# Kernel tuning notes

Measured on AMD Instinct MI355X. Metric: run time of the kernel, lower is better.

The kernel has to match this reference:

```python
import jax, jax.numpy as jnp
import numpy as np

B = 64          # batch_size
N_PER = 1000    # num_nodes per graph
NTOT = B * N_PER
H = 64          # hidden_gnn_dim


def _gcn_aggregate(x, senders, receivers, add_self_edges):
    """jraph.GraphConvolution aggregation with symmetric normalization.
    x: [NTOT, F] node features AFTER update_node_fn."""
    if add_self_edges:
        self_idx = jnp.arange(NTOT, dtype=senders.dtype)
        s = jnp.concatenate([senders, self_idx])
        r = jnp.concatenate([receivers, self_idx])
    else:
        s, r = senders, receivers
    ones = jnp.ones_like(s, dtype=x.dtype)
    deg_s = jax.ops.segment_sum(ones, s, num_segments=NTOT)
    deg_r = jax.ops.segment_sum(ones, r, num_segments=NTOT)
    x = x * jax.lax.rsqrt(jnp.maximum(deg_s, 1.0))[:, None]
    x = jax.ops.segment_sum(x[s], r, num_segments=NTOT)
    x = x * jax.lax.rsqrt(jnp.maximum(deg_r, 1.0))[:, None]
    return x


def setup_inputs() -> dict:
    key = jax.random.key(0)
    ks = jax.random.split(key, 12)
    n_edges = 1_000_000
    in_dim, fc, lat, out_dim = 64, 512, 64, 32
    flat = N_PER * H  # 64000

    def w(k, shape, fan_in):
        return jax.random.normal(k, shape, dtype=jnp.float32) / np.sqrt(fan_in)

    return {
        "nodes": jax.random.normal(ks[0], (NTOT, in_dim), dtype=jnp.float32),
        "senders": jax.random.randint(ks[1], (n_edges,), 0, NTOT),
        "receivers": jax.random.randint(ks[2], (n_edges,), 0, NTOT),
        "eps": jax.random.normal(ks[3], (B, lat), dtype=jnp.float32),
        "W_gcn1": w(ks[4], (in_dim, H), in_dim),
        "b_gcn1": jnp.zeros((H,), jnp.float32),
        "W_fc": w(ks[5], (flat, fc), flat),
        "b_fc": jnp.zeros((fc,), jnp.float32),
        "W_mean": w(ks[6], (fc, lat), fc),
        "b_mean": jnp.zeros((lat,), jnp.float32),
        "W_logstd": w(ks[7], (fc, lat), fc),
        "b_logstd": jnp.zeros((lat,), jnp.float32),
        "W_dec_fc": w(ks[8], (lat, flat), lat),
        "b_dec_fc": jnp.zeros((flat,), jnp.float32),
        "W_dec_out": w(ks[9], (H, out_dim), H),
        "b_dec_out": jnp.zeros((out_dim,), jnp.float32),
    }


def reference(nodes, senders, receivers, eps, W_gcn1, b_gcn1, W_fc, b_fc,
              W_mean, b_mean, W_logstd, b_logstd, W_dec_fc, b_dec_fc,
              W_dec_out, b_dec_out):
    # --- Encoder: GCN(update=Linear+relu, add_self_edges=True) ---
    h = jax.nn.relu(nodes @ W_gcn1 + b_gcn1)                 # [NTOT, H]
    h = _gcn_aggregate(h, senders, receivers, add_self_edges=True)
    x = h.reshape(B, N_PER * H)                              # flatten per graph
    x = jax.nn.relu(x @ W_fc + b_fc)                         # [B, fc]
    mean = x @ W_mean + b_mean                               # [B, lat]
    log_std = x @ W_logstd + b_logstd                        # [B, lat]
    # --- Reparameterization ---
    z = mean + jnp.exp(log_std) * eps                        # [B, lat]
    # --- Decoder ---
    d = jax.nn.relu(z @ W_dec_fc + b_dec_fc)                 # [B, N_PER*H]
    d = d.reshape(NTOT, H)
    d = d @ W_dec_out + b_dec_out                            # update_node_fn
    out_nodes = _gcn_aggregate(d, senders, receivers, add_self_edges=False)
    return mean, log_std, out_nodes
```

## Files before the change

### kernel.cpp

```cpp
#include <hip/hip_runtime.h>
#include <math.h>

#define NTOT 64000
#define HD   64
#define NB   64
#define FC   512
#define LAT  64
#define OUTD 32
#define GKC  256
#define NKB  250
#define NBH  64
#define NBUK 250
#define BSH  8

typedef __bf16 bf16x8 __attribute__((ext_vector_type(8)));
typedef float  f32x4  __attribute__((ext_vector_type(4)));

__device__ inline float bflo(unsigned u) { union {unsigned q; float f;} x; x.q = u << 16; return x.f; }
__device__ inline float bfhi(unsigned u) { union {unsigned q; float f;} x; x.q = u & 0xFFFF0000u; return x.f; }
__device__ inline unsigned pkbf(float lo, float hi) {
  __bf16 a = (__bf16)lo, b = (__bf16)hi;
  unsigned short ua, ub;
  __builtin_memcpy(&ua, &a, 2); __builtin_memcpy(&ub, &b, 2);
  return (unsigned)ua | ((unsigned)ub << 16);
}

__global__ __launch_bounds__(256) void k_hist(const int* __restrict__ s,
    const int* __restrict__ r, unsigned* __restrict__ partials, int nE) {
  __shared__ unsigned hist[16000];
  int arr = blockIdx.y;
  const int* idx = arr ? r : s;
  unsigned* base = partials + ((size_t)arr * NBH + blockIdx.x) * 16000;
  for (int u = threadIdx.x; u < 16000; u += 256) hist[u] = 0;
  __syncthreads();
  int chunk = (nE + NBH - 1) / NBH;
  int e0 = blockIdx.x * chunk;
  int e1 = min(e0 + chunk, nE);
  for (int e = e0 + threadIdx.x; e < e1; e += 256) {
    int i = idx[e];
    atomicAdd(&hist[i >> 2], 1u << ((i & 3) * 8));
  }
  __syncthreads();
  for (int u = threadIdx.x; u < 16000; u += 256) base[u] = hist[u];
}

__global__ __launch_bounds__(128) void k_sum(const unsigned* __restrict__ partials,
    int* __restrict__ dout, int* __restrict__ din) {
  int t = blockIdx.x * 128 + threadIdx.x;
  unsigned a = 0, b = 0;
  for (int bk = 0; bk < NBH; bk++) {
    a += partials[(size_t)bk * 16000 + t];
    b += partials[((size_t)NBH + bk) * 16000 + t];
  }
  int4 va = make_int4(a & 255, (a >> 8) & 255, (a >> 16) & 255, a >> 24);
  int4 vb = make_int4(b & 255, (b >> 8) & 255, (b >> 16) & 255, b >> 24);
  *reinterpret_cast<int4*>(dout + t * 4) = va;
  *reinterpret_cast<int4*>(din + t * 4) = vb;
}

__global__ void k_scan1(const int* __restrict__ din, int* __restrict__ rs,
                        int* __restrict__ bsums) {
  __shared__ int sm[256];
  int i = blockIdx.x * 256 + threadIdx.x;
  int v = din[i];
  sm[threadIdx.x] = v;
  __syncthreads();
  for (int d = 1; d < 256; d <<= 1) {
    int t = (threadIdx.x >= d) ? sm[threadIdx.x - d] : 0;
    __syncthreads();
    sm[threadIdx.x] += t;
    __syncthreads();
  }
  rs[i] = sm[threadIdx.x] - v;
  if (threadIdx.x == 255) bsums[blockIdx.x] = sm[255];
}

__global__ void k_scan2(int* __restrict__ rs, int* __restrict__ gcur,
                        const int* __restrict__ bsums, int nE) {
  __shared__ int sm[256];
  int bid = blockIdx.x, t = threadIdx.x;
  sm[t] = (t < bid) ? bsums[t] : 0;
  __syncthreads();
  for (int d = 128; d > 0; d >>= 1) {
    if (t < d) sm[t] += sm[t + d];
    __syncthreads();
  }
  int i = bid * 256 + t;
  int v = rs[i] + sm[0];
  rs[i] = v;
  if ((i & 255) == 0) gcur[i >> 8] = v;
  if (bid == 0 && t == 0) rs[NTOT] = nE;
}

__global__ __launch_bounds__(256) void k_bucket(const int* __restrict__ s,
    const int* __restrict__ r, int* __restrict__ gcur,
    unsigned* __restrict__ ebuf, int nE) {
  __shared__ int cnt[NBUK];
  __shared__ int base[NBUK];
  int tid = threadIdx.x;
  int chunk = (nE + gridDim.x - 1) / gridDim.x;
  int e0 = blockIdx.x * chunk;
  int e1 = min(e0 + chunk, nE);
  for (int u = tid; u < NBUK; u += 256) cnt[u] = 0;
  __syncthreads();
  for (int e = e0 + tid; e < e1; e += 256)
    atomicAdd(&cnt[r[e] >> BSH], 1);
  __syncthreads();
  for (int u = tid; u < NBUK; u += 256) {
    base[u] = atomicAdd(&gcur[u], cnt[u]);
    cnt[u] = 0;
  }
  __syncthreads();
  for (int e = e0 + tid; e < e1; e += 256) {
    int rr = r[e];
    int b = rr >> BSH;
    int off = atomicAdd(&cnt[b], 1);
    ebuf[base[b] + off] = ((unsigned)(rr & 255) << 16) | (unsigned)s[e];
  }
}

__global__ __launch_bounds__(256) void k_fill2(const unsigned* __restrict__ ebuf,
    const int* __restrict__ rs, int* __restrict__ csr) {
  __shared__ int cur[256];
  int b = blockIdx.x;
  int tid = threadIdx.x;
  int nbase = b << BSH;
  cur[tid] = rs[nbase + tid];
  __syncthreads();
  int e0 = rs[nbase];
  int e1 = rs[nbase + 256];
  for (int e = e0 + tid; e < e1; e += 256) {
    unsigned p = ebuf[e];
    int pos = atomicAdd(&cur[p >> 16], 1);
    csr[pos] = (int)(p & 0xFFFFu);
  }
}

__global__ __launch_bounds__(256) void k_node1(const float* __restrict__ nodes,
    const float* __restrict__ W1, const float* __restrict__ b1,
    const int* __restrict__ dout, __bf16* __restrict__ h1) {
  __shared__ float wsm[HD * HD];
  int tid = threadIdx.x;
  for (int u = tid; u < HD * HD; u += 256) wsm[u] = W1[u];
  __syncthreads();
  int node = blockIdx.x * 4 + (tid >> 6);
  int f = tid & 63;
  const float* xr = nodes + (size_t)node * HD;
  float acc = b1[f];
#pragma unroll 16
  for (int k = 0; k < HD; k++) acc = fmaf(xr[k], wsm[k * HD + f], acc);
  acc = fmaxf(acc, 0.f);
  h1[(size_t)node * HD + f] = (__bf16)(acc * rsqrtf((float)(dout[node] + 1)));
}

__global__ __launch_bounds__(256) void k_agg1(const unsigned* __restrict__ h1u,
    const int* __restrict__ rs, const int* __restrict__ csr,
    const int* __restrict__ din, unsigned* __restrict__ xbo) {
  int tid = threadIdx.x;
  int node = blockIdx.x * 8 + (tid >> 5);
  int f2 = tid & 31;
  int beg = rs[node], end = rs[node + 1];
  unsigned su = h1u[node * 32 + f2];
  float a0 = bflo(su), b0 = bfhi(su);
  float a1 = 0, b1 = 0, a2 = 0, b2 = 0, a3 = 0, b3 = 0;
  int e = beg;
  for (; e + 4 <= end; e += 4) {
    unsigned u0 = h1u[csr[e] * 32 + f2];
    unsigned u1 = h1u[csr[e + 1] * 32 + f2];
    unsigned u2 = h1u[csr[e + 2] * 32 + f2];
    unsigned u3 = h1u[csr[e + 3] * 32 + f2];
    a0 += bflo(u0); b0 += bfhi(u0);
    a1 += bflo(u1); b1 += bfhi(u1);
    a2 += bflo(u2); b2 += bfhi(u2);
    a3 += bflo(u3); b3 += bfhi(u3);
  }
  for (; e < end; e++) {
    unsigned u = h1u[csr[e] * 32 + f2];
    a1 += bflo(u); b1 += bfhi(u);
  }
  float sc = rsqrtf((float)(din[node] + 1));
  xbo[node * 32 + f2] = pkbf(((a0 + a1) + (a2 + a3)) * sc, ((b0 + b1) + (b2 + b3)) * sc);
}

__global__ __launch_bounds__(512) void k_gemm(const __bf16* __restrict__ xb,
    const float* __restrict__ Wfc, float* __restrict__ part) {
  __shared__ __align__(16) __bf16 As[64 * 264];
  int kb = blockIdx.x;
  int k0 = kb * GKC;
  int tid = threadIdx.x;
  for (int u = tid; u < 64 * 32; u += 512) {
    int row = u >> 5, c = u & 31;
    const uint4* src = reinterpret_cast<const uint4*>(xb + (size_t)row * 64000 + k0);
    reinterpret_cast<uint4*>(&As[row * 264])[c] = src[c];
  }
  __syncthreads();
  int w = tid >> 6, lane = tid & 63;
  int cw = lane & 15, kg = lane >> 4;
  const float* Bp = Wfc + ((size_t)k0 + kg * 8) * FC + w * 64 + cw;
  f32x4 acc[4][4];
#pragma unroll
  for (int mt = 0; mt < 4; mt++)
#pragma unroll
    for (int nt = 0; nt < 4; nt++) acc[mt][nt] = (f32x4){0.f, 0.f, 0.f, 0.f};

  for (int ks = 0; ks < 8; ks++) {
    bf16x8 bfrag[4];
#pragma unroll
    for (int nt = 0; nt < 4; nt++) {
      const float* bp = Bp + (size_t)ks * 32 * FC + nt * 16;
      bf16x8 bb;
#pragma unroll
      for (int b = 0; b < 8; b++) bb[b] = (__bf16)bp[(size_t)b * FC];
      bfrag[nt] = bb;
    }
    bf16x8 afrag[4];
#pragma unroll
    for (int mt = 0; mt < 4; mt++)
      afrag[mt] = *reinterpret_cast<const bf16x8*>(
          &As[(mt * 16 + cw) * 264 + ks * 32 + kg * 8]);
#pragma unroll
    for (int mt = 0; mt < 4; mt++)
#pragma unroll
      for (int nt = 0; nt < 4; nt++)
        acc[mt][nt] = __builtin_amdgcn_mfma_f32_16x16x32_bf16(
            afrag[mt], bfrag[nt], acc[mt][nt], 0, 0, 0);
  }
#pragma unroll
  for (int mt = 0; mt < 4; mt++)
#pragma unroll
    for (int nt = 0; nt < 4; nt++) {
      int col = w * 64 + nt * 16 + cw;
#pragma unroll
      for (int j = 0; j < 4; j++) {
        int row = mt * 16 + kg * 4 + j;
        part[((size_t)kb * 64 + row) * FC + col] = acc[mt][nt][j];
      }
    }
}

__global__ __launch_bounds__(256) void k_reduce(const float* __restrict__ part,
    const float* __restrict__ bfc, float* __restrict__ xf) {
  __shared__ float sm[256];
  int t = threadIdx.x;
  int i = blockIdx.x * 128 + (t & 127);
  int half = t >> 7;
  float sv = 0.f;
  int kb0 = half * (NKB / 2);
  int kb1 = kb0 + (NKB / 2);
  for (int kb = kb0; kb < kb1; kb++) sv += part[(size_t)kb * (NB * FC) + i];
  sm[t] = sv;
  __syncthreads();
  if (half == 0)
    xf[i] = fmaxf(sm[t] + sm[t + 128] + bfc[i & (FC - 1)], 0.f);
}

__global__ __launch_bounds__(256) void k_head(const float* __restrict__ xf,
    const float* __restrict__ Wm, const float* __restrict__ bm,
    const float* __restrict__ Wl, const float* __restrict__ bl,
    const float* __restrict__ eps, float* __restrict__ out_mean,
    float* __restrict__ out_logstd, float* __restrict__ z) {
  __shared__ float xr[FC];
  __shared__ float ps[4][LAT];
  __shared__ float zm[LAT];
  int b = blockIdx.x, t = threadIdx.x;
  for (int u = t; u < FC; u += 256) xr[u] = xf[b * FC + u];
  __syncthreads();
  int g = t >> 6;
  int l = t & 63;
  int h = g & 1;
  const float* W = (g < 2) ? Wm : Wl;
  float acc = 0.f;
  int kb = h * (FC / 2);
#pragma unroll 8
  for (int k = kb; k < kb + FC / 2; k++) acc = fmaf(xr[k], W[k * LAT + l], acc);
  ps[g][l] = acc;
  __syncthreads();
  float ls = 0.f;
  if (g == 0) {
    float m = ps[0][l] + ps[1][l] + bm[l];
    out_mean[b * 64 + l] = m;
    zm[l] = m;
  }
  if (g == 2) {
    ls = ps[2][l] + ps[3][l] + bl[l];
    out_logstd[b * 64 + l] = ls;
  }
  __syncthreads();
  if (g == 2) z[b * 64 + l] = zm[l] + expf(ls) * eps[b * 64 + l];
}

__global__ __launch_bounds__(256) void k_dec_fc(const float* __restrict__ z,
    const float* __restrict__ Wdf, const float* __restrict__ bdf,
    __bf16* __restrict__ dbuf) {
  __shared__ float zs[NB * LAT];
  int tid = threadIdx.x;
  for (int u = tid; u < NB * LAT; u += 256) zs[u] = z[u];
  __syncthreads();
  int j = blockIdx.x * 32 + (tid & 31);
  int b0 = (tid >> 5) * 8;
  float bias = bdf[j];
  float acc[8];
#pragma unroll
  for (int i = 0; i < 8; i++) acc[i] = bias;
  for (int k = 0; k < LAT; k++) {
    float w = Wdf[(size_t)k * 64000 + j];
#pragma unroll
    for (int i = 0; i < 8; i++) acc[i] = fmaf(zs[(b0 + i) * LAT + k], w, acc[i]);
  }
#pragma unroll
  for (int i = 0; i < 8; i++)
    dbuf[(size_t)(b0 + i) * 64000 + j] = (__bf16)fmaxf(acc[i], 0.f);
}

__global__ __launch_bounds__(256) void k_dec_out(const __bf16* __restrict__ dbuf,
    const float* __restrict__ Wdo, const float* __restrict__ bdo,
    const int* __restrict__ dout, __bf16* __restrict__ dds) {
  __shared__ float wsm[HD * OUTD];
  __shared__ float dr[8][HD];
  int tid = threadIdx.x;
  for (int u = tid; u < HD * OUTD; u += 256) wsm[u] = Wdo[u];
  int node0 = blockIdx.x * 8;
  {
    int nl = tid >> 5, k = tid & 31;
    dr[nl][k]      = (float)dbuf[(size_t)(node0 + nl) * HD + k];
    dr[nl][k + 32] = (float)dbuf[(size_t)(node0 + nl) * HD + k + 32];
  }
  __syncthreads();
  int nl = tid >> 5, f = tid & 31;
  int node = node0 + nl;
  float acc = bdo[f];
#pragma unroll 8
  for (int k = 0; k < HD; k++) acc = fmaf(dr[nl][k], wsm[k * OUTD + f], acc);
  dds[(size_t)node * OUTD + f] = (__bf16)(acc * rsqrtf(fmaxf((float)dout[node], 1.f)));
}

__global__ __launch_bounds__(256) void k_agg2(const unsigned* __restrict__ ddsu,
    const int* __restrict__ rs, const int* __restrict__ csr,
    const int* __restrict__ din, float* __restrict__ outn) {
  int tid = threadIdx.x;
  int node = blockIdx.x * 16 + (tid >> 4);
  int f2 = tid & 15;
  int beg = rs[node], end = rs[node + 1];
  float a0 = 0, b0 = 0, a1 = 0, b1 = 0, a2 = 0, b2 = 0, a3 = 0, b3 = 0;
  int e = beg;
  for (; e + 4 <= end; e += 4) {
    unsigned u0 = ddsu[csr[e] * 16 + f2];
    unsigned u1 = ddsu[csr[e + 1] * 16 + f2];
    unsigned u2 = ddsu[csr[e + 2] * 16 + f2];
    unsigned u3 = ddsu[csr[e + 3] * 16 + f2];
    a0 += bflo(u0); b0 += bfhi(u0);
    a1 += bflo(u1); b1 += bfhi(u1);
    a2 += bflo(u2); b2 += bfhi(u2);
    a3 += bflo(u3); b3 += bfhi(u3);
  }
  for (; e < end; e++) {
    unsigned u = ddsu[csr[e] * 16 + f2];
    a1 += bflo(u); b1 += bfhi(u);
  }
  float sc = rsqrtf(fmaxf((float)din[node], 1.f));
  float2 o = make_float2(((a0 + a1) + (a2 + a3)) * sc, ((b0 + b1) + (b2 + b3)) * sc);
  *reinterpret_cast<float2*>(outn + (size_t)node * 32 + f2 * 2) = o;
}

extern "C" void kernel_launch(void* const* d_in, const int* in_sizes, int n_in,
                              void* d_out, int out_size, void* d_ws, size_t ws_size,
                              hipStream_t stream) {
  const float* nodes   = (const float*)d_in[0];
  const int*   senders = (const int*)d_in[1];
  const int*   recvs   = (const int*)d_in[2];
  const float* eps     = (const float*)d_in[3];
  const float* W1      = (const float*)d_in[4];
  const float* b1      = (const float*)d_in[5];
  const float* Wfc     = (const float*)d_in[6];
  const float* bfc     = (const float*)d_in[7];
  const float* Wm      = (const float*)d_in[8];
  const float* bm      = (const float*)d_in[9];
  const float* Wl      = (const float*)d_in[10];
  const float* bl      = (const float*)d_in[11];
  const float* Wdf     = (const float*)d_in[12];
  const float* bdf     = (const float*)d_in[13];
  const float* Wdo     = (const float*)d_in[14];
  const float* bdo     = (const float*)d_in[15];
  int nE = in_sizes[1];

  char* w = (char*)d_ws;
  auto alloc = [&](size_t bytes) {
    char* p = w;
    w += (bytes + 255) & ~(size_t)255;
    return p;
  };
  int* deg_out   = (int*)alloc((size_t)NTOT * 4);
  int* deg_in    = (int*)alloc((size_t)NTOT * 4);
  int* row_start = (int*)alloc((size_t)(NTOT + 1) * 4);
  int* gcur      = (int*)alloc((size_t)NBUK * 4);
  int* bsums     = (int*)alloc(256 * 4);
  int* csr       = (int*)alloc((size_t)nE * 4);
  unsigned* ebuf = (unsigned*)alloc((size_t)nE * 4);
  __bf16* h1  = (__bf16*)alloc((size_t)NTOT * HD * 2);
  __bf16* xb  = (__bf16*)alloc((size_t)NTOT * HD * 2);
  float* part = (float*)alloc((size_t)NKB * NB * FC * 4);
  float* xf   = (float*)alloc((size_t)NB * FC * 4);
  float* z    = (float*)alloc((size_t)NB * LAT * 4);
  __bf16* dbuf = h1;
  __bf16* dds  = xb;
  unsigned* partials = (unsigned*)part;

  float* out_mean   = (float*)d_out;
  float* out_logstd = (float*)d_out + 4096;
  float* out_nodes  = (float*)d_out + 8192;

  k_hist<<<dim3(NBH, 2), 256, 0, stream>>>(senders, recvs, partials, nE);
  k_sum<<<125, 128, 0, stream>>>(partials, deg_out, deg_in);
  k_scan1<<<NTOT / 256, 256, 0, stream>>>(deg_in, row_start, bsums);
  k_scan2<<<NTOT / 256, 256, 0, stream>>>(row_start, gcur, bsums, nE);
  k_bucket<<<256, 256, 0, stream>>>(senders, recvs, gcur, ebuf, nE);
  k_fill2<<<NBUK, 256, 0, stream>>>(ebuf, row_start, csr);
  k_node1<<<NTOT / 4, 256, 0, stream>>>(nodes, W1, b1, deg_out, h1);
  k_agg1<<<NTOT / 8, 256, 0, stream>>>((const unsigned*)h1, row_start, csr, deg_in, (unsigned*)xb);
  k_gemm<<<NKB, 512, 0, stream>>>(xb, Wfc, part);
  k_reduce<<<NB * FC / 128, 256, 0, stream>>>(part, bfc, xf);
  k_head<<<NB, 256, 0, stream>>>(xf, Wm, bm, Wl, bl, eps, out_mean, out_logstd, z);
  k_dec_fc<<<64000 / 32, 256, 0, stream>>>(z, Wdf, bdf, dbuf);
  k_dec_out<<<NTOT / 8, 256, 0, stream>>>(dbuf, Wdo, bdo, deg_out, dds);
  k_agg2<<<NTOT / 16, 256, 0, stream>>>((const unsigned*)dds, row_start, csr, deg_in, out_nodes);
}
```

Before: 249.8 us.

## Stage W_fc tiles through LDS with register prefetch in FC GEMM

The FC GEMM kernel used to read W_fc directly from global memory as strided scalar loads, one per k row per lane. It now loads each 32x512 fp32 slab with coalesced float4 loads into registers, prefetching the next slab while the current one is consumed. The slab is stored to padded shared memory and the bf16 B fragments are built from LDS. NBH also grows from 64 to 128, which affects another kernel. The cost is extra LDS, two barriers per k-step and more register pressure.

```diff
diff --git a/kernel.cpp b/kernel.cpp
--- a/kernel.cpp
+++ b/kernel.cpp
@@ -9,7 +9,7 @@
 #define OUTD 32
 #define GKC  256
 #define NKB  250
-#define NBH  64
+#define NBH  128
 #define NBUK 250
 #define BSH  8
 
@@ -185,6 +185,7 @@
 __global__ __launch_bounds__(512) void k_gemm(const __bf16* __restrict__ xb,
     const float* __restrict__ Wfc, float* __restrict__ part) {
   __shared__ __align__(16) __bf16 As[64 * 264];
+  __shared__ __align__(16) float Bs[32 * 516];
   int kb = blockIdx.x;
   int k0 = kb * GKC;
   int tid = threadIdx.x;
@@ -193,10 +194,23 @@
     const uint4* src = reinterpret_cast<const uint4*>(xb + (size_t)row * 64000 + k0);
     reinterpret_cast<uint4*>(&As[row * 264])[c] = src[c];
   }
-  __syncthreads();
+  float4 breg[8];
+#pragma unroll
+  for (int i = 0; i < 8; i++) {
+    int q = tid + i * 512;
+    int row = q >> 7, c4 = q & 127;
+    breg[i] = *reinterpret_cast<const float4*>(Wfc + (size_t)(k0 + row) * FC + c4 * 4);
+  }
+#pragma unroll
+  for (int i = 0; i < 8; i++) {
+    int q = tid + i * 512;
+    int row = q >> 7, c4 = q & 127;
+    *reinterpret_cast<float4*>(&Bs[row * 516 + c4 * 4]) = breg[i];
+  }
+  __syncthreads();
+
   int w = tid >> 6, lane = tid & 63;
   int cw = lane & 15, kg = lane >> 4;
-  const float* Bp = Wfc + ((size_t)k0 + kg * 8) * FC + w * 64 + cw;
   f32x4 acc[4][4];
 #pragma unroll
   for (int mt = 0; mt < 4; mt++)
@@ -204,13 +218,23 @@
     for (int nt = 0; nt < 4; nt++) acc[mt][nt] = (f32x4){0.f, 0.f, 0.f, 0.f};
 
   for (int ks = 0; ks < 8; ks++) {
+    if (ks < 7) {
+#pragma unroll
+      for (int i = 0; i < 8; i++) {
+        int q = tid + i * 512;
+        int row = q >> 7, c4 = q & 127;
+        breg[i] = *reinterpret_cast<const float4*>(
+            Wfc + (size_t)(k0 + (ks + 1) * 32 + row) * FC + c4 * 4);
+      }
+    }
     bf16x8 bfrag[4];
 #pragma unroll
     for (int nt = 0; nt < 4; nt++) {
-      const float* bp = Bp + (size_t)ks * 32 * FC + nt * 16;
+      int col = w * 64 + nt * 16 + cw;
       bf16x8 bb;
 #pragma unroll
-      for (int b = 0; b < 8; b++) bb[b] = (__bf16)bp[(size_t)b * FC];
+      for (int j = 0; j < 8; j++)
+        bb[j] = (__bf16)Bs[(kg * 8 + j) * 516 + col];
       bfrag[nt] = bb;
     }
     bf16x8 afrag[4];
@@ -224,6 +248,16 @@
       for (int nt = 0; nt < 4; nt++)
         acc[mt][nt] = __builtin_amdgcn_mfma_f32_16x16x32_bf16(
             afrag[mt], bfrag[nt], acc[mt][nt], 0, 0, 0);
+    __syncthreads();
+    if (ks < 7) {
+#pragma unroll
+      for (int i = 0; i < 8; i++) {
+        int q = tid + i * 512;
+        int row = q >> 7, c4 = q & 127;
+        *reinterpret_cast<float4*>(&Bs[row * 516 + c4 * 4]) = breg[i];
+      }
+      __syncthreads();
+    }
   }
 #pragma unroll
   for (int mt = 0; mt < 4; mt++)
```

Result: slower. 287.7 us (+15.2%).
